# Optimization experiments

Hardware: AMD Instinct MI355X
Metric: run time of the kernel (lower is better)

Reference implementation:

```python
import jax, jax.numpy as jnp
import numpy as np

B, F, L, P = 64, 512, 512, 96
HT, HF = 8, 8  # temporal / feature attention heads
EPS_ATTN = 1e-6
EPS_LN = 1e-5
EPS_REVIN = 1e-5


def _layernorm(x, g, b):
    m = x.mean(axis=-1, keepdims=True)
    v = x.var(axis=-1, keepdims=True)
    return (x - m) / jnp.sqrt(v + EPS_LN) * g + b


def _lin_attn(x, Wq, bq, Wk, bk, Wv, bv, Wo, bo, H):
    # x: (B, N, D). Katharopoulos linear attention with elu+1 feature map.
    Bz, N, D = x.shape
    hd = D // H

    def proj(W, b):
        return (x @ W.T + b).reshape(Bz, N, H, hd).transpose(0, 2, 1, 3)  # (B,H,N,hd)

    Q = jax.nn.elu(proj(Wq, bq)) + 1.0
    K = jax.nn.elu(proj(Wk, bk)) + 1.0
    V = proj(Wv, bv)
    KV = jnp.einsum('bhnd,bhne->bhde', K, V)           # (B,H,hd,hd)
    out = jnp.einsum('bhnd,bhde->bhne', Q, KV)         # (B,H,N,hd)
    Z = K.sum(axis=2)                                  # (B,H,hd)
    norm = jnp.einsum('bhnd,bhd->bhn', Q, Z)[..., None] + EPS_ATTN
    out = (out / norm).transpose(0, 2, 1, 3).reshape(Bz, N, D)
    return out @ Wo.T + bo


def setup_inputs() -> dict:
    key = jax.random.key(0)
    ks = jax.random.split(key, 32)
    s = 0.1  # xavier-ish gain

    def w(k, shape, fan):
        return jax.random.normal(k, shape, dtype=jnp.float32) * (s / np.sqrt(fan))

    inp = {
        'x': jax.random.normal(ks[0], (B, F, L), dtype=jnp.float32),
        # RevIN affine
        'rg': jnp.ones((1, 1, F), jnp.float32),
        'rb': jnp.zeros((1, 1, F), jnp.float32),
        # LayerNorms
        'n1g': jnp.ones((F,), jnp.float32), 'n1b': jnp.zeros((F,), jnp.float32),
        'n2g': jnp.ones((L,), jnp.float32), 'n2b': jnp.zeros((L,), jnp.float32),
        # temporal attention (dim=F)
        'tWq': w(ks[1], (F, F), F), 'tbq': jnp.zeros((F,), jnp.float32),
        'tWk': w(ks[2], (F, F), F), 'tbk': jnp.zeros((F,), jnp.float32),
        'tWv': w(ks[3], (F, F), F), 'tbv': jnp.zeros((F,), jnp.float32),
        'tWo': w(ks[4], (F, F), F), 'tbo': jnp.zeros((F,), jnp.float32),
        # feature attention (dim=L)
        'fWq': w(ks[5], (L, L), L), 'fbq': jnp.zeros((L,), jnp.float32),
        'fWk': w(ks[6], (L, L), L), 'fbk': jnp.zeros((L,), jnp.float32),
        'fWv': w(ks[7], (L, L), L), 'fbv': jnp.zeros((L,), jnp.float32),
        'fWo': w(ks[8], (L, L), L), 'fbo': jnp.zeros((L,), jnp.float32),
        # individual per-feature Linear bank: seq_len -> pred_len
        'Wlin': w(ks[9], (F, P, L), L), 'blin': jnp.zeros((F, P), jnp.float32),
        # projector F -> 1
        'Wproj': w(ks[10], (1, F), F), 'bproj': jnp.zeros((1,), jnp.float32),
    }
    return inp


def reference(x, rg, rb, n1g, n1b,
              tWq, tbq, tWk, tbk, tWv, tbv, tWo, tbo,
              n2g, n2b,
              fWq, fbq, fWk, fbk, fWv, fbv, fWo, fbo,
              Wlin, blin, Wproj, bproj):
    # (B, F, L) -> (B, L, F)
    h = x.transpose(0, 2, 1)
    # RevIN norm (stats detached, std is unbiased like torch.std)
    mean = jax.lax.stop_gradient(h.mean(axis=1, keepdims=True))
    std = jax.lax.stop_gradient(jnp.std(h, axis=1, keepdims=True, ddof=1) + EPS_REVIN)
    h = (h - mean) / std * rg + rb

    # Dual linear attention
    r = h
    h = _layernorm(h, n1g, n1b)
    h = _lin_attn(h, tWq, tbq, tWk, tbk, tWv, tbv, tWo, tbo, HT) + r
    h = h.transpose(0, 2, 1)  # (B, F, L)
    r = h
    h = _layernorm(h, n2g, n2b)
    h = _lin_attn(h, fWq, fbq, fWk, fbk, fWv, fbv, fWo, fbo, HF) + r
    # (module transposes back to (B,L,F) then LinearCrypto permutes to (B,F,L);
    #  we stay in (B,F,L))

    # individual per-feature linear: seq_len -> pred_len
    y = jnp.einsum('bfl,fpl->bfp', h, Wlin) + blin[None]  # (B,F,P)
    y = y.transpose(0, 2, 1)                              # (B,P,F)
    # RevIN denorm
    y = (y - rb) / rg
    y = y * std + mean
    # projector F -> 1
    out = y @ Wproj.T + bproj  # (B,P,1)
    return out[..., 0]
```

## Files before the change

### kernel.cpp

```cpp
#include <hip/hip_runtime.h>
#include <hip/hip_bf16.h>
#include <cstdint>
#include <cstddef>


#define EPS_ATTN 1e-6f
#define EPS_LN   1e-5f
#define EPS_REVIN 1e-5f

typedef __attribute__((ext_vector_type(8))) short bf16x8;
typedef __attribute__((ext_vector_type(4))) float f32x4;
typedef __attribute__((ext_vector_type(8))) unsigned short u16x8;

__device__ __forceinline__ float bf2f(unsigned short u) {
  unsigned int x = ((unsigned int)u) << 16;
  return __builtin_bit_cast(float, x);
}
__device__ __forceinline__ unsigned short f2bf(float f) {
  __hip_bfloat16 h = __float2bfloat16(f);
  return __builtin_bit_cast(unsigned short, h);
}
__device__ __forceinline__ void gload16(const void* g, void* l) {
  __builtin_amdgcn_global_load_lds(
      (const __attribute__((address_space(1))) void*)g,
      (__attribute__((address_space(3))) void*)l, 16, 0, 0);
}

__global__ __launch_bounds__(256) void revin_xn_k(const float* __restrict__ x,
                                                  const float* __restrict__ rg,
                                                  const float* __restrict__ rb,
                                                  float* __restrict__ meanb,
                                                  float* __restrict__ stdb,
                                                  unsigned short* __restrict__ xn) {
  int wid = threadIdx.x >> 6, lane = threadIdx.x & 63;
  int row = blockIdx.x * 4 + wid;
  const float* xr = x + (size_t)row * 512 + lane * 8;
  float4 a = *(const float4*)xr;
  float4 c = *(const float4*)(xr + 4);
  float s1 = a.x + a.y + a.z + a.w + c.x + c.y + c.z + c.w;
  float s2 = a.x * a.x + a.y * a.y + a.z * a.z + a.w * a.w +
             c.x * c.x + c.y * c.y + c.z * c.z + c.w * c.w;
#pragma unroll
  for (int off = 1; off < 64; off <<= 1) { s1 += __shfl_xor(s1, off); s2 += __shfl_xor(s2, off); }
  float m = s1 * (1.f / 512.f);
  float var = fmaxf((s2 - 512.f * m * m) * (1.f / 511.f), 0.f);
  float sd = sqrtf(var) + EPS_REVIN;
  int f = row & 511;
  float sc = rg[f] / sd;
  float of = rb[f] - m * sc;
  u16x8 o;
  o[0] = f2bf(a.x * sc + of); o[1] = f2bf(a.y * sc + of);
  o[2] = f2bf(a.z * sc + of); o[3] = f2bf(a.w * sc + of);
  o[4] = f2bf(c.x * sc + of); o[5] = f2bf(c.y * sc + of);
  o[6] = f2bf(c.z * sc + of); o[7] = f2bf(c.w * sc + of);
  *(u16x8*)(xn + (size_t)row * 512 + lane * 8) = o;
  if (lane == 0) { meanb[row] = m; stdb[row] = sd; }
}

__global__ __launch_bounds__(256) void transpose_bf_k(const unsigned short* __restrict__ xn,
                                                      unsigned short* __restrict__ h1) {
  __shared__ float T[64][65];
  int b = blockIdx.z, f0 = blockIdx.y * 64, l0 = blockIdx.x * 64;
  int tid = threadIdx.x;
  int fr = tid >> 3, l8 = (tid & 7) * 8;
#pragma unroll
  for (int p = 0; p < 2; ++p) {
    int f = p * 32 + fr;
    u16x8 v = *(const u16x8*)(xn + ((size_t)(b * 512 + f0 + f)) * 512 + l0 + l8);
#pragma unroll
    for (int j = 0; j < 8; ++j) T[l8 + j][f] = bf2f(v[j]);
  }
  __syncthreads();
#pragma unroll
  for (int p = 0; p < 2; ++p) {
    int l = p * 32 + (tid >> 3), f8 = (tid & 7) * 8;
    u16x8 o;
#pragma unroll
    for (int j = 0; j < 8; ++j) o[j] = f2bf(T[l][f8 + j]);
    *(u16x8*)(h1 + ((size_t)(b * 512 + l0 + l)) * 512 + f0 + f8) = o;
  }
}

__global__ __launch_bounds__(256) void ln_k(const unsigned short* __restrict__ in,
                                            const float* __restrict__ g,
                                            const float* __restrict__ bq,
                                            unsigned short* __restrict__ o16) {
  int row = blockIdx.x * 4 + (threadIdx.x >> 6);
  int lane = threadIdx.x & 63;
  u16x8 u = *(const u16x8*)(in + (size_t)row * 512 + lane * 8);
  float v[8];
#pragma unroll
  for (int j = 0; j < 8; ++j) v[j] = bf2f(u[j]);
  float s1 = 0.f, s2 = 0.f;
#pragma unroll
  for (int j = 0; j < 8; ++j) { s1 += v[j]; s2 += v[j] * v[j]; }
#pragma unroll
  for (int off = 1; off < 64; off <<= 1) { s1 += __shfl_xor(s1, off); s2 += __shfl_xor(s2, off); }
  float m = s1 * (1.f / 512.f);
  float var = fmaxf(s2 * (1.f / 512.f) - m * m, 0.f);
  float iv = 1.f / sqrtf(var + EPS_LN);
  float4 g0 = *(const float4*)(g + lane * 8);
  float4 g1 = *(const float4*)(g + lane * 8 + 4);
  float4 b0 = *(const float4*)(bq + lane * 8);
  float4 b1 = *(const float4*)(bq + lane * 8 + 4);
  u16x8 o;
  o[0] = f2bf((v[0] - m) * iv * g0.x + b0.x);
  o[1] = f2bf((v[1] - m) * iv * g0.y + b0.y);
  o[2] = f2bf((v[2] - m) * iv * g0.z + b0.z);
  o[3] = f2bf((v[3] - m) * iv * g0.w + b0.w);
  o[4] = f2bf((v[4] - m) * iv * g1.x + b1.x);
  o[5] = f2bf((v[5] - m) * iv * g1.y + b1.y);
  o[6] = f2bf((v[6] - m) * iv * g1.z + b1.z);
  o[7] = f2bf((v[7] - m) * iv * g1.w + b1.w);
  *(u16x8*)(o16 + (size_t)row * 512 + lane * 8) = o;
}

__global__ __launch_bounds__(256) void wconv_k(const float* w0, const float* w1,
                                               const float* w2, const float* w3,
                                               const float* w4, const float* w5,
                                               const float* w6, const float* w7,
                                               unsigned short* __restrict__ out) {
  const float* srcs[8] = {w0, w1, w2, w3, w4, w5, w6, w7};
  const float* s = srcs[blockIdx.y];
  size_t idx = (size_t)blockIdx.x * 2048 + threadIdx.x * 8;
  float4 v0 = *(const float4*)(s + idx);
  float4 v1 = *(const float4*)(s + idx + 4);
  u16x8 o;
  o[0] = f2bf(v0.x); o[1] = f2bf(v0.y); o[2] = f2bf(v0.z); o[3] = f2bf(v0.w);
  o[4] = f2bf(v1.x); o[5] = f2bf(v1.y); o[6] = f2bf(v1.z); o[7] = f2bf(v1.w);
  *(u16x8*)(out + (size_t)blockIdx.y * 262144 + idx) = o;
}

__device__ __forceinline__ void gemm_core(const unsigned short* __restrict__ A,
                                          const unsigned short* __restrict__ W,
                                          unsigned short* smem,
                                          f32x4 (&acc)[4][4],
                                          int m0, int wrow, int tid) {
  const int w = tid >> 6, lane = tid & 63;
  const int wr = w >> 1, wc = w & 1;
  const int r8 = lane >> 3, s8 = lane & 7, gslot = s8 ^ r8;
  const unsigned short* Ag = A + (size_t)(m0 + w * 32 + r8) * 512 + gslot * 8;
  const unsigned short* Wg = W + (size_t)(wrow + w * 32 + r8) * 512 + gslot * 8;
  unsigned short* Asw = smem + w * 2048;
  unsigned short* Bsw = smem + 8192 + w * 2048;
  for (int k0 = 0; k0 < 512; k0 += 64) {
#pragma unroll
    for (int c = 0; c < 4; ++c) {
      gload16(Ag + (size_t)c * 8 * 512 + k0, Asw + c * 512);
      gload16(Wg + (size_t)c * 8 * 512 + k0, Bsw + c * 512);
    }
    __syncthreads();
#pragma unroll
    for (int s = 0; s < 2; ++s) {
      bf16x8 fa[4], fb[4];
#pragma unroll
      for (int i = 0; i < 4; ++i) {
        int ra = wr * 64 + i * 16 + (lane & 15);
        int sa = (s * 4 + (lane >> 4)) ^ (ra & 7);
        fa[i] = *(const bf16x8*)&smem[ra * 64 + sa * 8];
        int rb = wc * 64 + i * 16 + (lane & 15);
        int sb = (s * 4 + (lane >> 4)) ^ (rb & 7);
        fb[i] = *(const bf16x8*)&smem[8192 + rb * 64 + sb * 8];
      }
#pragma unroll
      for (int i = 0; i < 4; ++i)
#pragma unroll
        for (int j = 0; j < 4; ++j)
          acc[i][j] = __builtin_amdgcn_mfma_f32_16x16x32_bf16(fa[i], fb[j], acc[i][j], 0, 0, 0);
    }
    __syncthreads();
  }
}

template <int TRANS, int ACT, int RES>
__device__ __forceinline__ void gemm_epilogue(f32x4 (&acc)[4][4],
                                              unsigned short* Cs,
                                              const float* __restrict__ bias,
                                              const unsigned short* __restrict__ resid,
                                              unsigned short* __restrict__ out,
                                              int m0, int n0, int tid) {
  const int w = tid >> 6, lane = tid & 63;
  const int wr = w >> 1, wc = w & 1;
  const int ro = (lane >> 4) * 4, c16 = lane & 15;
#pragma unroll
  for (int j = 0; j < 4; ++j) {
    int nl = wc * 64 + j * 16 + c16;
    float bi = bias[n0 + nl];
#pragma unroll
    for (int i = 0; i < 4; ++i) {
      int ml = wr * 64 + i * 16 + ro;
#pragma unroll
      for (int r = 0; r < 4; ++r) {
        float v = acc[i][j][r] + bi;
        if constexpr (ACT) v = (v > 0.f) ? v + 1.f : __expf(v);
        if constexpr (TRANS) Cs[nl * 136 + ml + r] = f2bf(v);
        else                 Cs[(ml + r) * 136 + nl] = f2bf(v);
      }
    }
  }
  __syncthreads();
  size_t rowbase; int colbase;
  if constexpr (TRANS) { rowbase = (size_t)((m0 >> 9) * 512 + n0); colbase = m0 & 511; }
  else                 { rowbase = (size_t)m0; colbase = n0; }
#pragma unroll
  for (int c = 0; c < 8; ++c) {
    int idx = c * 256 + tid;
    int rr = idx >> 4, c8 = (idx & 15) * 8;
    u16x8 v = *(const u16x8*)&Cs[rr * 136 + c8];
    size_t gaddr = (rowbase + rr) * 512 + colbase + c8;
    if constexpr (RES) {
      u16x8 rv = *(const u16x8*)(resid + gaddr);
#pragma unroll
      for (int q = 0; q < 8; ++q) v[q] = f2bf(bf2f(v[q]) + bf2f(rv[q]));
    }
    *(u16x8*)(out + gaddr) = v;
  }
}

template <int TRANS, int ACT, int RES>
__global__ __launch_bounds__(256, 4) void gemm_std_k(const unsigned short* __restrict__ A,
                                                     const unsigned short* __restrict__ W,
                                                     const float* __restrict__ bias,
                                                     const unsigned short* __restrict__ resid,
                                                     unsigned short* __restrict__ out) {
  __shared__ unsigned short smem[17408] __attribute__((aligned(16)));
  const int tid = threadIdx.x;
  const int bid = blockIdx.x;
  const int nb = (bid & 7) * 128 + (bid >> 3);
  const int m0 = (nb >> 2) * 128;
  const int n0 = (nb & 3) * 128;
  f32x4 acc[4][4] = {};
  gemm_core(A, W, smem, acc, m0, n0, tid);
  gemm_epilogue<TRANS, ACT, RES>(acc, smem, bias, resid, out, m0, n0, tid);
}

__global__ __launch_bounds__(256, 4) void gemm_qkv3_k(const unsigned short* __restrict__ A,
                                                      const unsigned short* __restrict__ Wqkv,
                                                      const float* __restrict__ bq,
                                                      const float* __restrict__ bk,
                                                      const float* __restrict__ bv,
                                                      unsigned short* __restrict__ Q,
                                                      unsigned short* __restrict__ K,
                                                      unsigned short* __restrict__ V) {
  __shared__ unsigned short smem[17408] __attribute__((aligned(16)));
  const int tid = threadIdx.x;
  const unsigned int bid = blockIdx.x;
  const unsigned int nb = (bid & 7) * 384 + (bid >> 3);
  const int mi = nb / 12, ni = nb % 12;
  const int m0 = mi * 128;
  const int mat = ni >> 2;
  const int n0 = (ni & 3) * 128;
  f32x4 acc[4][4] = {};
  gemm_core(A, Wqkv, smem, acc, m0, mat * 512 + n0, tid);

  const float* bias = (mat == 0) ? bq : (mat == 1) ? bk : bv;
  unsigned short* out = (mat == 0) ? Q : (mat == 1) ? K : V;
  const bool trans = (mat > 0);
  const bool act = (mat < 2);

  const int w = tid >> 6, lane = tid & 63;
  const int wr = w >> 1, wc = w & 1;
  const int ro = (lane >> 4) * 4, c16 = lane & 15;
  unsigned short* Cs = smem;
#pragma unroll
  for (int j = 0; j < 4; ++j) {
    int nl = wc * 64 + j * 16 + c16;
    float bi = bias[n0 + nl];
#pragma unroll
    for (int i = 0; i < 4; ++i) {
      int ml = wr * 64 + i * 16 + ro;
#pragma unroll
      for (int r = 0; r < 4; ++r) {
        float v = acc[i][j][r] + bi;
        if (act) v = (v > 0.f) ? v + 1.f : __expf(v);
        int row = trans ? nl : (ml + r);
        int col = trans ? (ml + r) : nl;
        Cs[row * 136 + col] = f2bf(v);
      }
    }
  }
  __syncthreads();
  size_t rowbase = trans ? (size_t)((m0 >> 9) * 512 + n0) : (size_t)m0;
  int colbase = trans ? (m0 & 511) : n0;
#pragma unroll
  for (int c = 0; c < 8; ++c) {
    int idx = c * 256 + tid;
    int rr = idx >> 4, c8 = (idx & 15) * 8;
    u16x8 v = *(const u16x8*)&Cs[rr * 136 + c8];
    *(u16x8*)(out + (rowbase + rr) * 512 + colbase + c8) = v;
  }
}

__global__ __launch_bounds__(256) void kv_mfma_k(const unsigned short* __restrict__ KT,
                                                 const unsigned short* __restrict__ VT,
                                                 unsigned short* __restrict__ KVTo,
                                                 float* __restrict__ Zo) {
  int bh = blockIdx.x;
  int tid = threadIdx.x, w = tid >> 6, lane = tid & 63;
  int r16 = lane & 15, g = lane >> 4;
  const unsigned short* vb = VT + ((size_t)bh * 64 + w * 16 + r16) * 512 + g * 8;
  const unsigned short* kb = KT + ((size_t)bh * 64 + r16) * 512 + g * 8;
  f32x4 acc[4] = {};
  float zp[4] = {};
  for (int n0 = 0; n0 < 512; n0 += 32) {
    bf16x8 vf = *(const bf16x8*)(vb + n0);
#pragma unroll
    for (int j = 0; j < 4; ++j) {
      bf16x8 kf = *(const bf16x8*)(kb + (size_t)j * 16 * 512 + n0);
#pragma unroll
      for (int q = 0; q < 8; ++q) zp[j] += bf2f((unsigned short)kf[q]);
      acc[j] = __builtin_amdgcn_mfma_f32_16x16x32_bf16(vf, kf, acc[j], 0, 0, 0);
    }
  }
  int e = w * 16 + g * 4;
  unsigned short* kvo = KVTo + (size_t)bh * 4096;
#pragma unroll
  for (int j = 0; j < 4; ++j)
#pragma unroll
    for (int r = 0; r < 4; ++r)
      kvo[(size_t)(e + r) * 64 + j * 16 + r16] = f2bf(acc[j][r]);
#pragma unroll
  for (int j = 0; j < 4; ++j) {
    zp[j] += __shfl_xor(zp[j], 16);
    zp[j] += __shfl_xor(zp[j], 32);
  }
  if (w == 0 && lane < 16) {
#pragma unroll
    for (int j = 0; j < 4; ++j) Zo[(size_t)bh * 64 + j * 16 + lane] = zp[j];
  }
}

__global__ __launch_bounds__(512) void attn_mfma_k(unsigned short* __restrict__ Q16,
                                                   const unsigned short* __restrict__ KVT,
                                                   const float* __restrict__ Z) {
  __shared__ unsigned short kvs[32768] __attribute__((aligned(16)));
  __shared__ float Zs[512];
  int tid = threadIdx.x;
  int b = blockIdx.x >> 2;
  int m0 = blockIdx.x * 128;
  const unsigned short* kg = KVT + (size_t)b * 32768;
#pragma unroll
  for (int t = 0; t < 8; ++t) {
    int c = tid + t * 512;
    int e = (c >> 3) & 63;
    u16x8 v = *(const u16x8*)(kg + (size_t)c * 8);
    *(u16x8*)((char*)kvs + ((c * 16) ^ ((e & 7) << 4))) = v;
  }
  Zs[tid] = Z[(size_t)b * 512 + tid];
  __syncthreads();

  int w = tid >> 6, lane = tid & 63;
  int r16 = lane & 15, g = lane >> 4;
  unsigned short* qrow = Q16 + (size_t)(m0 + w * 16 + r16) * 512;
  int orow0 = m0 + w * 16 + g * 4;

  for (int h = 0; h < 8; ++h) {
    bf16x8 q0 = *(const bf16x8*)(qrow + h * 64 + g * 8);
    bf16x8 q1 = *(const bf16x8*)(qrow + h * 64 + 32 + g * 8);
    const float* zh = Zs + h * 64;
    float np = 0.f;
#pragma unroll
    for (int q = 0; q < 8; ++q) np = fmaf(bf2f((unsigned short)q0[q]), zh[g * 8 + q], np);
#pragma unroll
    for (int q = 0; q < 8; ++q) np = fmaf(bf2f((unsigned short)q1[q]), zh[32 + g * 8 + q], np);

    f32x4 acc[4] = {};
#pragma unroll
    for (int j = 0; j < 4; ++j) {
      int e = j * 16 + r16;
      int byte0 = h * 8192 + e * 128;
      int sw = (e & 7) << 4;
      bf16x8 k0 = *(const bf16x8*)((char*)kvs + ((byte0 + g * 16) ^ sw));
      bf16x8 k1 = *(const bf16x8*)((char*)kvs + ((byte0 + 64 + g * 16) ^ sw));
      acc[j] = __builtin_amdgcn_mfma_f32_16x16x32_bf16(q0, k0, acc[j], 0, 0, 0);
      acc[j] = __builtin_amdgcn_mfma_f32_16x16x32_bf16(q1, k1, acc[j], 0, 0, 0);
    }
    np += __shfl_xor(np, 16);
    np += __shfl_xor(np, 32);
    float inv = 1.f / (np + EPS_ATTN);
    float inv4[4];
#pragma unroll
    for (int r = 0; r < 4; ++r) inv4[r] = __shfl(inv, g * 4 + r);
#pragma unroll
    for (int j = 0; j < 4; ++j)
#pragma unroll
      for (int r = 0; r < 4; ++r)
        Q16[(size_t)(orow0 + r) * 512 + h * 64 + j * 16 + r16] = f2bf(acc[j][r] * inv4[r]);
  }
}

__global__ __launch_bounds__(256) void feat_linear_k(const unsigned short* __restrict__ h3,
                                                     const float* __restrict__ Wlin,
                                                     const float* __restrict__ blin,
                                                     float* __restrict__ Y) {
  __shared__ unsigned short As[64 * 64] __attribute__((aligned(16)));
  __shared__ unsigned short Bs[96 * 64] __attribute__((aligned(16)));
  const int f = blockIdx.x;
  const int tid = threadIdx.x;
  const int w = tid >> 6, lane = tid & 63;
  const int r16 = lane & 15, g = lane >> 4;
  const int r8 = lane >> 3, s8 = lane & 7, gs = s8 ^ r8;

  f32x4 acc[6] = {};
  for (int k0 = 0; k0 < 512; k0 += 64) {
#pragma unroll
    for (int c = 0; c < 2; ++c) {
      int row = w * 16 + c * 8 + r8;
      gload16(h3 + ((size_t)row * 512 + f) * 512 + k0 + gs * 8,
              As + (w * 16 + c * 8) * 64);
    }
#pragma unroll
    for (int it = 0; it < 3; ++it) {
      int idx = it * 256 + tid;
      int pp = idx >> 3, sl = idx & 7;
      const float* src = Wlin + ((size_t)f * 96 + pp) * 512 + k0 + sl * 8;
      float4 v0 = *(const float4*)src;
      float4 v1 = *(const float4*)(src + 4);
      u16x8 o;
      o[0] = f2bf(v0.x); o[1] = f2bf(v0.y); o[2] = f2bf(v0.z); o[3] = f2bf(v0.w);
      o[4] = f2bf(v1.x); o[5] = f2bf(v1.y); o[6] = f2bf(v1.z); o[7] = f2bf(v1.w);
      *(u16x8*)&Bs[pp * 64 + (sl ^ (pp & 7)) * 8] = o;
    }
    __syncthreads();
#pragma unroll
    for (int s = 0; s < 2; ++s) {
      int arow = w * 16 + r16;
      bf16x8 fa = *(const bf16x8*)&As[arow * 64 + (((s * 4 + g) ^ (arow & 7)) * 8)];
#pragma unroll
      for (int n = 0; n < 6; ++n) {
        int brow = n * 16 + r16;
        bf16x8 fb = *(const bf16x8*)&Bs[brow * 64 + (((s * 4 + g) ^ (brow & 7)) * 8)];
        acc[n] = __builtin_amdgcn_mfma_f32_16x16x32_bf16(fa, fb, acc[n], 0, 0, 0);
      }
    }
    __syncthreads();
  }
  const int b0 = w * 16 + g * 4;
#pragma unroll
  for (int n = 0; n < 6; ++n) {
    float bi = blin[f * 96 + n * 16 + r16];
#pragma unroll
    for (int r = 0; r < 4; ++r)
      Y[((size_t)(b0 + r) * 512 + f) * 96 + n * 16 + r16] = acc[n][r] + bi;
  }
}

__global__ __launch_bounds__(256) void final_out_k(const float* __restrict__ Y,
                                                   const float* __restrict__ meanb,
                                                   const float* __restrict__ stdb,
                                                   const float* __restrict__ rg,
                                                   const float* __restrict__ rb,
                                                   const float* __restrict__ Wproj,
                                                   const float* __restrict__ bproj,
                                                   float* __restrict__ out) {
  int b = blockIdx.x;
  __shared__ float cs[512];
  __shared__ float kred[4];
  int t = threadIdx.x;
  float kpart = 0.f;
  for (int f = t; f < 512; f += 256) {
    float sd = stdb[b * 512 + f], mn = meanb[b * 512 + f];
    float g = rg[f], rbv = rb[f], wp = Wproj[f];
    float c = wp * sd / g;
    cs[f] = c;
    kpart += wp * mn - c * rbv;
  }
#pragma unroll
  for (int off = 32; off; off >>= 1) kpart += __shfl_down(kpart, off);
  int wid = t >> 6, lane = t & 63;
  if (lane == 0) kred[wid] = kpart;
  __syncthreads();
  float K = kred[0] + kred[1] + kred[2] + kred[3] + bproj[0];
  if (t < 96) {
    float acc = 0.f;
    for (int f = 0; f < 512; ++f) acc = fmaf(cs[f], Y[((size_t)b * 512 + f) * 96 + t], acc);
    out[b * 96 + t] = acc + K;
  }
}

extern "C" void kernel_launch(void* const* d_in, const int* in_sizes, int n_in,
                              void* d_out, int out_size, void* d_ws, size_t ws_size,
                              hipStream_t stream) {
  const float* x    = (const float*)d_in[0];
  const float* rg   = (const float*)d_in[1];
  const float* rb   = (const float*)d_in[2];
  const float* n1g  = (const float*)d_in[3];
  const float* n1b  = (const float*)d_in[4];
  const float* n2g  = (const float*)d_in[5];
  const float* n2b  = (const float*)d_in[6];
  const float* tWq  = (const float*)d_in[7];
  const float* tbq  = (const float*)d_in[8];
  const float* tWk  = (const float*)d_in[9];
  const float* tbk  = (const float*)d_in[10];
  const float* tWv  = (const float*)d_in[11];
  const float* tbv  = (const float*)d_in[12];
  const float* tWo  = (const float*)d_in[13];
  const float* tbo  = (const float*)d_in[14];
  const float* fWq  = (const float*)d_in[15];
  const float* fbq  = (const float*)d_in[16];
  const float* fWk  = (const float*)d_in[17];
  const float* fbk  = (const float*)d_in[18];
  const float* fWv  = (const float*)d_in[19];
  const float* fbv  = (const float*)d_in[20];
  const float* fWo  = (const float*)d_in[21];
  const float* fbo  = (const float*)d_in[22];
  const float* Wlin = (const float*)d_in[23];
  const float* blin = (const float*)d_in[24];
  const float* Wprj = (const float*)d_in[25];
  const float* bprj = (const float*)d_in[26];
  float* out = (float*)d_out;

  const size_t SZ = (size_t)64 * 512 * 512;
  char* p = (char*)d_ws;
  unsigned short* xn  = (unsigned short*)p; p += SZ * 2;
  unsigned short* h1  = (unsigned short*)p; p += SZ * 2;
  unsigned short* h2  = (unsigned short*)p; p += SZ * 2;
  unsigned short* h3  = (unsigned short*)p; p += SZ * 2;
  unsigned short* abf = (unsigned short*)p; p += SZ * 2;
  unsigned short* q16 = (unsigned short*)p; p += SZ * 2;
  unsigned short* k16 = (unsigned short*)p; p += SZ * 2;
  unsigned short* v16 = (unsigned short*)p; p += SZ * 2;
  unsigned short* wbf = (unsigned short*)p; p += (size_t)8 * 262144 * 2;
  unsigned short* kvt = (unsigned short*)p; p += (size_t)512 * 4096 * 2;
  float* z     = (float*)p;         p += (size_t)512 * 64 * 4;
  float* meanb = (float*)p;         p += 32768 * 4;
  float* stdb  = (float*)p;         p += 32768 * 4;
  float* ybuf  = (float*)abf;

  wconv_k<<<dim3(128, 8), 256, 0, stream>>>(tWq, tWk, tWv, tWo, fWq, fWk, fWv, fWo, wbf);
  revin_xn_k<<<8192, 256, 0, stream>>>(x, rg, rb, meanb, stdb, xn);
  transpose_bf_k<<<dim3(8, 8, 64), 256, 0, stream>>>(xn, h1);

  ln_k<<<8192, 256, 0, stream>>>(h1, n1g, n1b, abf);
  gemm_qkv3_k<<<3072, 256, 0, stream>>>(abf, wbf, tbq, tbk, tbv, q16, k16, v16);
  kv_mfma_k<<<512, 256, 0, stream>>>(k16, v16, kvt, z);
  attn_mfma_k<<<256, 512, 0, stream>>>(q16, kvt, z);
  gemm_std_k<1, 0, 1><<<1024, 256, 0, stream>>>(q16, wbf + 3 * 262144, tbo, xn, h2);

  ln_k<<<8192, 256, 0, stream>>>(h2, n2g, n2b, abf);
  gemm_qkv3_k<<<3072, 256, 0, stream>>>(abf, wbf + 4 * 262144, fbq, fbk, fbv, q16, k16, v16);
  kv_mfma_k<<<512, 256, 0, stream>>>(k16, v16, kvt, z);
  attn_mfma_k<<<256, 512, 0, stream>>>(q16, kvt, z);
  gemm_std_k<0, 0, 1><<<1024, 256, 0, stream>>>(q16, wbf + 7 * 262144, fbo, h2, h3);

  feat_linear_k<<<512, 256, 0, stream>>>(h3, Wlin, blin, ybuf);
  final_out_k<<<64, 256, 0, stream>>>(ybuf, meanb, stdb, rg, rb, Wprj, bprj, out);
}
```

Baseline: 382.9 us.

## Fuse transpose with first LayerNorm, stagger GEMM k-order, MFMA key sums

Replaces the separate transpose and first LayerNorm kernels with one kernel that transposes a 32-row slab in LDS, normalizes it and writes bf16. This removes a full intermediate buffer round trip through HBM. The GEMM k-loop now starts at a per-block rotated offset, spreading concurrent blocks across different K slices to reduce memory hot-spotting. The per-head key sum Z is computed with an extra MFMA against a ones vector instead of scalar adds and shuffles, which adds matrix work but drops VALU work.

```diff
diff --git a/kernel.cpp b/kernel.cpp
--- a/kernel.cpp
+++ b/kernel.cpp
@@ -57,27 +57,66 @@
   if (lane == 0) { meanb[row] = m; stdb[row] = sd; }
 }
 
-__global__ __launch_bounds__(256) void transpose_bf_k(const unsigned short* __restrict__ xn,
-                                                      unsigned short* __restrict__ h1) {
-  __shared__ float T[64][65];
-  int b = blockIdx.z, f0 = blockIdx.y * 64, l0 = blockIdx.x * 64;
-  int tid = threadIdx.x;
-  int fr = tid >> 3, l8 = (tid & 7) * 8;
-#pragma unroll
-  for (int p = 0; p < 2; ++p) {
-    int f = p * 32 + fr;
-    u16x8 v = *(const u16x8*)(xn + ((size_t)(b * 512 + f0 + f)) * 512 + l0 + l8);
-#pragma unroll
-    for (int j = 0; j < 8; ++j) T[l8 + j][f] = bf2f(v[j]);
+__global__ __launch_bounds__(256) void tln_k(const unsigned short* __restrict__ xn,
+                                             const float* __restrict__ g,
+                                             const float* __restrict__ bq,
+                                             unsigned short* __restrict__ o16) {
+  __shared__ unsigned short Ts[32][528] __attribute__((aligned(16)));
+  const int b = blockIdx.y, l0 = blockIdx.x * 32;
+  const int tid = threadIdx.x;
+#pragma unroll
+  for (int it = 0; it < 8; ++it) {
+    int idx = it * 256 + tid;
+    int f = idx >> 2, lc = (idx & 3) * 8;
+    u16x8 v = *(const u16x8*)(xn + ((size_t)b * 512 + f) * 512 + l0 + lc);
+#pragma unroll
+    for (int j = 0; j < 8; ++j) Ts[lc + j][f] = v[j];
   }
   __syncthreads();
-#pragma unroll
-  for (int p = 0; p < 2; ++p) {
-    int l = p * 32 + (tid >> 3), f8 = (tid & 7) * 8;
+  const int l = tid >> 3, q = tid & 7;
+  float s1 = 0.f, s2 = 0.f;
+#pragma unroll
+  for (int i = 0; i < 8; ++i) {
+    int c = (i + q) & 7;
+    bf16x8 t = *(const bf16x8*)&Ts[l][q * 64 + c * 8];
+#pragma unroll
+    for (int j = 0; j < 8; ++j) {
+      float x = bf2f((unsigned short)t[j]);
+      s1 += x; s2 += x * x;
+    }
+  }
+#pragma unroll
+  for (int off = 1; off < 8; off <<= 1) { s1 += __shfl_xor(s1, off); s2 += __shfl_xor(s2, off); }
+  float m = s1 * (1.f / 512.f);
+  float var = fmaxf(s2 * (1.f / 512.f) - m * m, 0.f);
+  float iv = 1.f / sqrtf(var + EPS_LN);
+#pragma unroll
+  for (int i = 0; i < 8; ++i) {
+    int c = (i + q) & 7;
+    int f8 = q * 64 + c * 8;
+    bf16x8 t = *(const bf16x8*)&Ts[l][f8];
+    float4 g0 = *(const float4*)(g + f8);
+    float4 g1 = *(const float4*)(g + f8 + 4);
+    float4 b0 = *(const float4*)(bq + f8);
+    float4 b1 = *(const float4*)(bq + f8 + 4);
     u16x8 o;
-#pragma unroll
-    for (int j = 0; j < 8; ++j) o[j] = f2bf(T[l][f8 + j]);
-    *(u16x8*)(h1 + ((size_t)(b * 512 + l0 + l)) * 512 + f0 + f8) = o;
+    o[0] = f2bf((bf2f((unsigned short)t[0]) - m) * iv * g0.x + b0.x);
+    o[1] = f2bf((bf2f((unsigned short)t[1]) - m) * iv * g0.y + b0.y);
+    o[2] = f2bf((bf2f((unsigned short)t[2]) - m) * iv * g0.z + b0.z);
+    o[3] = f2bf((bf2f((unsigned short)t[3]) - m) * iv * g0.w + b0.w);
+    o[4] = f2bf((bf2f((unsigned short)t[4]) - m) * iv * g1.x + b1.x);
+    o[5] = f2bf((bf2f((unsigned short)t[5]) - m) * iv * g1.y + b1.y);
+    o[6] = f2bf((bf2f((unsigned short)t[6]) - m) * iv * g1.z + b1.z);
+    o[7] = f2bf((bf2f((unsigned short)t[7]) - m) * iv * g1.w + b1.w);
+    *(u16x8*)&Ts[l][f8] = o;
+  }
+  __syncthreads();
+#pragma unroll
+  for (int it = 0; it < 8; ++it) {
+    int idx = it * 256 + tid;
+    int ll = idx >> 6, f8 = (idx & 63) * 8;
+    u16x8 v = *(const u16x8*)&Ts[ll][f8];
+    *(u16x8*)(o16 + ((size_t)b * 512 + l0 + ll) * 512 + f8) = v;
   }
 }
 
@@ -135,7 +174,7 @@
                                           const unsigned short* __restrict__ W,
                                           unsigned short* smem,
                                           f32x4 (&acc)[4][4],
-                                          int m0, int wrow, int tid) {
+                                          int m0, int wrow, int tid, int koff) {
   const int w = tid >> 6, lane = tid & 63;
   const int wr = w >> 1, wc = w & 1;
   const int r8 = lane >> 3, s8 = lane & 7, gslot = s8 ^ r8;
@@ -143,7 +182,8 @@
   const unsigned short* Wg = W + (size_t)(wrow + w * 32 + r8) * 512 + gslot * 8;
   unsigned short* Asw = smem + w * 2048;
   unsigned short* Bsw = smem + 8192 + w * 2048;
-  for (int k0 = 0; k0 < 512; k0 += 64) {
+  for (int kk = 0; kk < 8; ++kk) {
+    const int k0 = ((kk + koff) & 7) * 64;
 #pragma unroll
     for (int c = 0; c < 4; ++c) {
       gload16(Ag + (size_t)c * 8 * 512 + k0, Asw + c * 512);
@@ -230,7 +270,7 @@
   const int m0 = (nb >> 2) * 128;
   const int n0 = (nb & 3) * 128;
   f32x4 acc[4][4] = {};
-  gemm_core(A, W, smem, acc, m0, n0, tid);
+  gemm_core(A, W, smem, acc, m0, n0, tid, (bid >> 3) & 7);
   gemm_epilogue<TRANS, ACT, RES>(acc, smem, bias, resid, out, m0, n0, tid);
 }
 
@@ -251,7 +291,7 @@
   const int mat = ni >> 2;
   const int n0 = (ni & 3) * 128;
   f32x4 acc[4][4] = {};
-  gemm_core(A, Wqkv, smem, acc, m0, mat * 512 + n0, tid);
+  gemm_core(A, Wqkv, smem, acc, m0, mat * 512 + n0, tid, (bid >> 3) & 7);
 
   const float* bias = (mat == 0) ? bq : (mat == 1) ? bk : bv;
   unsigned short* out = (mat == 0) ? Q : (mat == 1) ? K : V;
@@ -300,16 +340,17 @@
   int r16 = lane & 15, g = lane >> 4;
   const unsigned short* vb = VT + ((size_t)bh * 64 + w * 16 + r16) * 512 + g * 8;
   const unsigned short* kb = KT + ((size_t)bh * 64 + r16) * 512 + g * 8;
+  const short ob = (short)0x3F80;
+  const bf16x8 onesf = {ob, ob, ob, ob, ob, ob, ob, ob};
   f32x4 acc[4] = {};
-  float zp[4] = {};
+  f32x4 zacc[4] = {};
   for (int n0 = 0; n0 < 512; n0 += 32) {
     bf16x8 vf = *(const bf16x8*)(vb + n0);
 #pragma unroll
     for (int j = 0; j < 4; ++j) {
       bf16x8 kf = *(const bf16x8*)(kb + (size_t)j * 16 * 512 + n0);
-#pragma unroll
-      for (int q = 0; q < 8; ++q) zp[j] += bf2f((unsigned short)kf[q]);
       acc[j] = __builtin_amdgcn_mfma_f32_16x16x32_bf16(vf, kf, acc[j], 0, 0, 0);
+      zacc[j] = __builtin_amdgcn_mfma_f32_16x16x32_bf16(onesf, kf, zacc[j], 0, 0, 0);
     }
   }
   int e = w * 16 + g * 4;
@@ -319,14 +360,9 @@
 #pragma unroll
     for (int r = 0; r < 4; ++r)
       kvo[(size_t)(e + r) * 64 + j * 16 + r16] = f2bf(acc[j][r]);
-#pragma unroll
-  for (int j = 0; j < 4; ++j) {
-    zp[j] += __shfl_xor(zp[j], 16);
-    zp[j] += __shfl_xor(zp[j], 32);
-  }
-  if (w == 0 && lane < 16) {
-#pragma unroll
-    for (int j = 0; j < 4; ++j) Zo[(size_t)bh * 64 + j * 16 + lane] = zp[j];
+  if (w == 0 && g == 0) {
+#pragma unroll
+    for (int j = 0; j < 4; ++j) Zo[(size_t)bh * 64 + j * 16 + r16] = zacc[j][0];
   }
 }
 
@@ -513,7 +549,6 @@
   const size_t SZ = (size_t)64 * 512 * 512;
   char* p = (char*)d_ws;
   unsigned short* xn  = (unsigned short*)p; p += SZ * 2;
-  unsigned short* h1  = (unsigned short*)p; p += SZ * 2;
   unsigned short* h2  = (unsigned short*)p; p += SZ * 2;
   unsigned short* h3  = (unsigned short*)p; p += SZ * 2;
   unsigned short* abf = (unsigned short*)p; p += SZ * 2;
@@ -529,9 +564,8 @@
 
   wconv_k<<<dim3(128, 8), 256, 0, stream>>>(tWq, tWk, tWv, tWo, fWq, fWk, fWv, fWo, wbf);
   revin_xn_k<<<8192, 256, 0, stream>>>(x, rg, rb, meanb, stdb, xn);
-  transpose_bf_k<<<dim3(8, 8, 64), 256, 0, stream>>>(xn, h1);
-
-  ln_k<<<8192, 256, 0, stream>>>(h1, n1g, n1b, abf);
+
+  tln_k<<<dim3(16, 64), 256, 0, stream>>>(xn, n1g, n1b, abf);
   gemm_qkv3_k<<<3072, 256, 0, stream>>>(abf, wbf, tbq, tbk, tbv, q16, k16, v16);
   kv_mfma_k<<<512, 256, 0, stream>>>(k16, v16, kvt, z);
   attn_mfma_k<<<256, 512, 0, stream>>>(q16, kvt, z);
```

After: 381.4 us. No clear change (-0.4%).
